# Kernel tuning notes

Hardware: AMD Instinct MI355X
Metric: run time of the kernel (lower is better)

The kernel has to match this reference:

```python
import jax, jax.numpy as jnp
import numpy as np

N_NODES = 100000
N_EDGES = 1600000
IN_DIM = 128
HID = 64


def _init_linear(key, fan_in, fan_out):
    kw, kb = jax.random.split(key)
    bound = 1.0 / np.sqrt(fan_in)
    W = jax.random.uniform(kw, (fan_in, fan_out), jnp.float32, -bound, bound)
    b = jax.random.uniform(kb, (fan_out,), jnp.float32, -bound, bound)
    return W, b


def setup_inputs() -> dict:
    key = jax.random.key(0)
    ks = jax.random.split(key, 6)
    x = jax.random.normal(ks[0], (N_NODES, IN_DIM), jnp.float32)
    edge_index = jax.random.randint(ks[1], (2, N_EDGES), 0, N_NODES, jnp.int64)
    W_pre, b_pre = _init_linear(ks[2], IN_DIM, HID)
    W1, b1 = _init_linear(ks[3], HID, HID)
    W2, b2 = _init_linear(ks[4], HID, HID)
    W3, b3 = _init_linear(ks[5], HID, HID)
    return {"x": x, "edge_index": edge_index, "W_pre": W_pre, "b_pre": b_pre,
            "W1": W1, "b1": b1, "W2": W2, "b2": b2, "W3": W3, "b3": b3}


def _gcn_layer(h, src, dst, dinv, W, b):
    # PyG GCNConv: h' = D^{-1/2} (A + I) D^{-1/2} (h W) + b, deg from A+I
    n = h.shape[0]
    hw = h @ W                                  # [N, out]
    norm = dinv[src] * dinv[dst]                # [E]
    msg = hw[src] * norm[:, None]               # gather + scale  [E, out]
    agg = jax.ops.segment_sum(msg, dst, num_segments=n)  # scatter-add
    agg = agg + hw * (dinv * dinv)[:, None]     # self-loop term (norm = dinv_i^2)
    return agg + b


def reference(x, edge_index, W_pre, b_pre, W1, b1, W2, b2, W3, b3):
    src, dst = edge_index[0], edge_index[1]
    n = x.shape[0]
    # degree of A + I (self loops added, as in GCNConv default)
    deg = jax.ops.segment_sum(jnp.ones(src.shape[0], x.dtype), dst, num_segments=n) + 1.0
    dinv = jax.lax.rsqrt(deg)

    h = x @ W_pre + b_pre                       # feature_pre linear
    h = jax.nn.relu(_gcn_layer(h, src, dst, dinv, W1, b1))  # dropout is identity in eval
    h = jax.nn.relu(_gcn_layer(h, src, dst, dinv, W2, b2))
    h = _gcn_layer(h, src, dst, dinv, W3, b3)
    # F.normalize(p=2, dim=-1) with eps=1e-12
    nrm = jnp.linalg.norm(h, axis=-1, keepdims=True)
    return h / jnp.maximum(nrm, 1e-12)
```

## Files before the change

### kernel.cpp

```cpp
#include <hip/hip_runtime.h>

#define N_NODES 100000
#define N_EDGES 1600000
#define IN_DIM 128
#define HID 64
#define NB 782
#define NT64 1563
#define NGROUP 25000

typedef __attribute__((ext_vector_type(8))) _Float16 h8v;
typedef __attribute__((ext_vector_type(4))) float f4v;

struct Args {
  const float* x; const int* ei;
  const float* Wp; const float* bp;
  const float* W1; const float* b1;
  const float* W2; const float* b2;
  const float* W3; const float* b3;
  float* out;
  _Float16* bufA16; _Float16* hw16;
  int* pairs; int* csr; int* offs; float* dinv;
  int* bsz; int* bboff; int* bcur;
  _Float16* WpH; _Float16* WpL; _Float16* W1H; _Float16* W1L;
  _Float16* W2H; _Float16* W2L; _Float16* W3H; _Float16* W3L;
};

__device__ __forceinline__ void d_split(const float* __restrict__ W,
                                        _Float16* __restrict__ hi,
                                        _Float16* __restrict__ lo, int K, int i) {
  int k = i >> 6, n = i & 63;
  float v = W[i];
  _Float16 h = (_Float16)v;
  float r = v - (float)h;
  hi[n * K + k] = h;
  lo[n * K + k] = (_Float16)r;
}

__global__ __launch_bounds__(256) void f_prep(Args a) {
  int blk = blockIdx.x, t = threadIdx.x;
  if (blk < 32) d_split(a.Wp, a.WpH, a.WpL, IN_DIM, blk * 256 + t);
  else if (blk < 48) d_split(a.W1, a.W1H, a.W1L, HID, (blk - 32) * 256 + t);
  else if (blk < 64) d_split(a.W2, a.W2H, a.W2L, HID, (blk - 48) * 256 + t);
  else d_split(a.W3, a.W3H, a.W3L, HID, (blk - 64) * 256 + t);
}

__global__ __launch_bounds__(256) void f_bhist(Args a) {
  __shared__ int cnt[NB];
  int t = threadIdx.x;
  for (int i = t; i < NB; i += 256) cnt[i] = 0;
  __syncthreads();
  int e0 = blockIdx.x * 8192, e1 = min(e0 + 8192, N_EDGES);
  for (int e = e0 + t; e < e1; e += 256)
    atomicAdd(&cnt[a.ei[N_EDGES + e] >> 7], 1);
  __syncthreads();
  for (int i = t; i < NB; i += 256)
    if (cnt[i]) atomicAdd(&a.bsz[i], cnt[i]);
}

__global__ __launch_bounds__(256) void f_bscan(Args a) {
  __shared__ int sm[256];
  int t = threadIdx.x;
  int c[4];
  int idx0 = t * 4;
#pragma unroll
  for (int j = 0; j < 4; ++j) c[j] = (idx0 + j < NB) ? a.bsz[idx0 + j] : 0;
  int tsum = c[0] + c[1] + c[2] + c[3];
  int val = tsum;
  sm[t] = val;
  __syncthreads();
  for (int off = 1; off < 256; off <<= 1) {
    int u = (t >= off) ? sm[t - off] : 0;
    __syncthreads();
    val += u;
    sm[t] = val;
    __syncthreads();
  }
  int excl = val - tsum;
#pragma unroll
  for (int j = 0; j < 4; ++j) {
    int idx = idx0 + j;
    if (idx < NB) { a.bboff[idx] = excl; a.bcur[idx] = excl; }
    excl += c[j];
  }
  if (t == 255) a.bboff[NB] = val;
}

__global__ __launch_bounds__(256) void f_partition(Args a) {
  __shared__ int cnt[NB];
  __shared__ int base[NB];
  int t = threadIdx.x;
  for (int i = t; i < NB; i += 256) cnt[i] = 0;
  __syncthreads();
  int e0 = blockIdx.x * 8192, e1 = min(e0 + 8192, N_EDGES);
  for (int e = e0 + t; e < e1; e += 256)
    atomicAdd(&cnt[a.ei[N_EDGES + e] >> 7], 1);
  __syncthreads();
  for (int i = t; i < NB; i += 256) {
    int c = cnt[i];
    base[i] = c ? atomicAdd(&a.bcur[i], c) : 0;
    cnt[i] = 0;
  }
  __syncthreads();
  for (int e = e0 + t; e < e1; e += 256) {
    int s = a.ei[e];
    int d = a.ei[N_EDGES + e];
    int b = d >> 7;
    int r = atomicAdd(&cnt[b], 1);
    a.pairs[base[b] + r] = ((d & 127) << 17) | s;
  }
}

__global__ __launch_bounds__(256) void f_csrdeg(Args a) {
  __shared__ int ldeg[128];
  __shared__ int sc[128];
  __shared__ int lcur[128];
  int t = threadIdx.x;
  int b = blockIdx.x;
  int node0 = b << 7;
  int nloc = min(128, N_NODES - node0);
  int beg = a.bboff[b], end = a.bboff[b + 1];
  if (t < 128) ldeg[t] = 0;
  __syncthreads();
  for (int i = beg + t; i < end; i += 256)
    atomicAdd(&ldeg[(a.pairs[i] >> 17) & 127], 1);
  __syncthreads();
  int dv = (t < 128) ? ldeg[t] : 0;
  if (t < 128) sc[t] = dv;
  __syncthreads();
  for (int off = 1; off < 128; off <<= 1) {
    int u = (t >= off && t < 128) ? sc[t - off] : 0;
    __syncthreads();
    if (t < 128) sc[t] += u;
    __syncthreads();
  }
  if (t < nloc) {
    int o = beg + sc[t] - dv;
    a.offs[node0 + t] = o;
    lcur[t] = o;
    a.dinv[node0 + t] = rsqrtf((float)dv + 1.0f);
  }
  if (b == NB - 1 && t == 0) a.offs[N_NODES] = N_EDGES;
  __syncthreads();
  for (int i = beg + t; i < end; i += 256) {
    int p = a.pairs[i];
    int pos = atomicAdd(&lcur[(p >> 17) & 127], 1);
    a.csr[pos] = p & 131071;
  }
}

__global__ __launch_bounds__(256) void f_gemm_pre(Args a) {
  const int K = IN_DIM;
  int wave = threadIdx.x >> 6;
  int lane = threadIdx.x & 63;
  int fi = lane & 15;
  int quad = lane >> 4;
  int r0 = blockIdx.x * 64 + wave * 16;
  int row_l = r0 + fi;
  if (row_l >= N_NODES) row_l = N_NODES - 1;
  const float* xp = a.x + (size_t)row_l * K + quad * 8;

  f4v acc[4];
#pragma unroll
  for (int ct = 0; ct < 4; ++ct) acc[ct] = (f4v){0.f, 0.f, 0.f, 0.f};

#pragma unroll
  for (int k0 = 0; k0 < K; k0 += 32) {
    f4v xa = *(const f4v*)(xp + k0);
    f4v xb = *(const f4v*)(xp + k0 + 4);
    h8v ah, al;
#pragma unroll
    for (int j = 0; j < 4; ++j) {
      _Float16 h = (_Float16)xa[j];
      ah[j] = h;
      al[j] = (_Float16)(xa[j] - (float)h);
    }
#pragma unroll
    for (int j = 0; j < 4; ++j) {
      _Float16 h = (_Float16)xb[j];
      ah[4 + j] = h;
      al[4 + j] = (_Float16)(xb[j] - (float)h);
    }
    const _Float16* whp = a.WpH + (size_t)fi * K + k0 + quad * 8;
    const _Float16* wlp = a.WpL + (size_t)fi * K + k0 + quad * 8;
#pragma unroll
    for (int ct = 0; ct < 4; ++ct) {
      h8v bh = *(const h8v*)(whp + (size_t)ct * 16 * K);
      h8v bl = *(const h8v*)(wlp + (size_t)ct * 16 * K);
      acc[ct] = __builtin_amdgcn_mfma_f32_16x16x32_f16(ah, bh, acc[ct], 0, 0, 0);
      acc[ct] = __builtin_amdgcn_mfma_f32_16x16x32_f16(al, bh, acc[ct], 0, 0, 0);
      acc[ct] = __builtin_amdgcn_mfma_f32_16x16x32_f16(ah, bl, acc[ct], 0, 0, 0);
    }
  }
#pragma unroll
  for (int ct = 0; ct < 4; ++ct) {
    float bv = a.bp[ct * 16 + fi];
#pragma unroll
    for (int j = 0; j < 4; ++j) {
      int orow = r0 + quad * 4 + j;
      if (orow < N_NODES)
        a.bufA16[(size_t)orow * HID + ct * 16 + fi] = (_Float16)(acc[ct][j] + bv);
    }
  }
}

__global__ __launch_bounds__(256) void f_gemm64(Args a, const _Float16* __restrict__ Wh,
                                                const _Float16* __restrict__ Wl) {
  const int K = HID;
  int wave = threadIdx.x >> 6;
  int lane = threadIdx.x & 63;
  int fi = lane & 15;
  int quad = lane >> 4;
  int r0 = blockIdx.x * 64 + wave * 16;
  int row_l = r0 + fi;
  if (row_l >= N_NODES) row_l = N_NODES - 1;
  const _Float16* xp = a.bufA16 + (size_t)row_l * K + quad * 8;

  f4v acc[4];
#pragma unroll
  for (int ct = 0; ct < 4; ++ct) acc[ct] = (f4v){0.f, 0.f, 0.f, 0.f};

#pragma unroll
  for (int k0 = 0; k0 < K; k0 += 32) {
    h8v av = *(const h8v*)(xp + k0);
    const _Float16* whp = Wh + (size_t)fi * K + k0 + quad * 8;
    const _Float16* wlp = Wl + (size_t)fi * K + k0 + quad * 8;
#pragma unroll
    for (int ct = 0; ct < 4; ++ct) {
      h8v bh = *(const h8v*)(whp + (size_t)ct * 16 * K);
      h8v bl = *(const h8v*)(wlp + (size_t)ct * 16 * K);
      acc[ct] = __builtin_amdgcn_mfma_f32_16x16x32_f16(av, bh, acc[ct], 0, 0, 0);
      acc[ct] = __builtin_amdgcn_mfma_f32_16x16x32_f16(av, bl, acc[ct], 0, 0, 0);
    }
  }
#pragma unroll
  for (int ct = 0; ct < 4; ++ct) {
#pragma unroll
    for (int j = 0; j < 4; ++j) {
      int orow = r0 + quad * 4 + j;
      if (orow < N_NODES)
        a.hw16[(size_t)orow * HID + ct * 16 + fi] = (_Float16)acc[ct][j];
    }
  }
}

template <int MODE>
__device__ __forceinline__ void d_agg(int grp, const _Float16* __restrict__ hw,
                                      const int* __restrict__ offs,
                                      const int* __restrict__ csr,
                                      const float* __restrict__ dinv,
                                      const float* __restrict__ bias,
                                      _Float16* __restrict__ out16,
                                      float* __restrict__ out32) {
  int node = grp * 4 + (threadIdx.x >> 6);
  int lane = threadIdx.x & 63;
  int oct = lane >> 3;
  int fi = lane & 7;
  float di = dinv[node];
  int beg = offs[node];
  int end = offs[node + 1];

  float acc[8];
#pragma unroll
  for (int c = 0; c < 8; ++c) acc[c] = 0.f;

  if (oct == 0) {
    h8v hv = *(const h8v*)(hw + (size_t)node * HID + fi * 8);
    float w = di * di;
#pragma unroll
    for (int c = 0; c < 8; ++c) acc[c] += (float)hv[c] * w;
  }
  for (int e0 = beg + oct; e0 < end; e0 += 32) {
    int ss[4];
    float ww[4];
#pragma unroll
    for (int j = 0; j < 4; ++j) {
      int e = e0 + 8 * j;
      bool v = e < end;
      int s = csr[v ? e : beg];
      ss[j] = v ? s : node;
      ww[j] = v ? di : 0.0f;
    }
#pragma unroll
    for (int j = 0; j < 4; ++j) ww[j] *= dinv[ss[j]];
    h8v hv[4];
#pragma unroll
    for (int j = 0; j < 4; ++j)
      hv[j] = *(const h8v*)(hw + (size_t)ss[j] * HID + fi * 8);
#pragma unroll
    for (int j = 0; j < 4; ++j)
#pragma unroll
      for (int c = 0; c < 8; ++c) acc[c] += (float)hv[j][c] * ww[j];
  }
#pragma unroll
  for (int c = 0; c < 8; ++c) {
    float v = acc[c];
    v += __shfl_xor(v, 8);
    v += __shfl_xor(v, 16);
    v += __shfl_xor(v, 32);
    acc[c] = v;
  }
  if (oct == 0) {
#pragma unroll
    for (int c = 0; c < 8; ++c) acc[c] += bias[fi * 8 + c];
    if (MODE == 0) {
      h8v o;
#pragma unroll
      for (int c = 0; c < 8; ++c) o[c] = (_Float16)fmaxf(acc[c], 0.f);
      *(h8v*)(out16 + (size_t)node * HID + fi * 8) = o;
    } else {
      float ss = 0.f;
#pragma unroll
      for (int c = 0; c < 8; ++c) ss += acc[c] * acc[c];
      ss += __shfl_xor(ss, 1);
      ss += __shfl_xor(ss, 2);
      ss += __shfl_xor(ss, 4);
      float sc = 1.0f / fmaxf(sqrtf(ss), 1e-12f);
      f4v o0 = {acc[0] * sc, acc[1] * sc, acc[2] * sc, acc[3] * sc};
      f4v o1 = {acc[4] * sc, acc[5] * sc, acc[6] * sc, acc[7] * sc};
      *(f4v*)(out32 + (size_t)node * HID + fi * 8) = o0;
      *(f4v*)(out32 + (size_t)node * HID + fi * 8 + 4) = o1;
    }
  }
}

__global__ __launch_bounds__(256) void f_agg_relu(Args a, const float* bias) {
  d_agg<0>(blockIdx.x, a.hw16, a.offs, a.csr, a.dinv, bias, a.bufA16, nullptr);
}

__global__ __launch_bounds__(256) void f_agg_norm(Args a) {
  d_agg<1>(blockIdx.x, a.hw16, a.offs, a.csr, a.dinv, a.b3, nullptr, a.out);
}

extern "C" void kernel_launch(void* const* d_in, const int* in_sizes, int n_in,
                              void* d_out, int out_size, void* d_ws, size_t ws_size,
                              hipStream_t stream) {
  char* ws = (char*)d_ws;
  Args a;
  a.x  = (const float*)d_in[0];
  a.ei = (const int*)d_in[1];
  a.Wp = (const float*)d_in[2];  a.bp = (const float*)d_in[3];
  a.W1 = (const float*)d_in[4];  a.b1 = (const float*)d_in[5];
  a.W2 = (const float*)d_in[6];  a.b2 = (const float*)d_in[7];
  a.W3 = (const float*)d_in[8];  a.b3 = (const float*)d_in[9];
  a.out  = (float*)d_out;
  a.bufA16 = (_Float16*)(ws + 0);
  a.hw16   = (_Float16*)(ws + 12800000);
  a.pairs  = (int*)(ws + 25600000);
  a.csr    = (int*)(ws + 32000000);
  a.offs   = (int*)(ws + 38400000);
  a.dinv   = (float*)(ws + 38800016);
  a.bsz    = (int*)(ws + 39200016);
  a.bboff  = (int*)(ws + 39203152);
  a.bcur   = (int*)(ws + 39206288);
  a.WpH = (_Float16*)(ws + 39210000);
  a.WpL = (_Float16*)(ws + 39226384);
  a.W1H = (_Float16*)(ws + 39242768);
  a.W1L = (_Float16*)(ws + 39250960);
  a.W2H = (_Float16*)(ws + 39259152);
  a.W2L = (_Float16*)(ws + 39267344);
  a.W3H = (_Float16*)(ws + 39275536);
  a.W3L = (_Float16*)(ws + 39283728);

  (void)hipMemsetAsync(a.bsz, 0, NB * sizeof(int), stream);
  f_prep<<<80, 256, 0, stream>>>(a);
  f_bhist<<<196, 256, 0, stream>>>(a);
  f_bscan<<<1, 256, 0, stream>>>(a);
  f_partition<<<196, 256, 0, stream>>>(a);
  f_csrdeg<<<NB, 256, 0, stream>>>(a);
  f_gemm_pre<<<NT64, 256, 0, stream>>>(a);
  f_gemm64<<<NT64, 256, 0, stream>>>(a, a.W1H, a.W1L);
  f_agg_relu<<<NGROUP, 256, 0, stream>>>(a, a.b1);
  f_gemm64<<<NT64, 256, 0, stream>>>(a, a.W2H, a.W2L);
  f_agg_relu<<<NGROUP, 256, 0, stream>>>(a, a.b2);
  f_gemm64<<<NT64, 256, 0, stream>>>(a, a.W3H, a.W3L);
  f_agg_norm<<<NGROUP, 256, 0, stream>>>(a);
}
```

Measured before the change: 383.2 us.

## Process two row tiles per wave and stage pre-GEMM weights in LDS

Each wave now computes 32 rows (two 16-row tiles) instead of 16, which halves the block count for the dense GEMMs. The weight fragments are loaded once and reused across both tiles, held in registers for the 64-wide GEMMs and in swizzled shared memory for the input projection. The next tile's activations are prefetched while the current tile's MFMAs run. The aim is to cut redundant weight loads from global memory and hide load latency, at the cost of more registers and LDS per block and fewer blocks.

```diff
diff --git a/kernel.cpp b/kernel.cpp
--- a/kernel.cpp
+++ b/kernel.cpp
@@ -5,7 +5,7 @@
 #define IN_DIM 128
 #define HID 64
 #define NB 782
-#define NT64 1563
+#define NBLK_GEMM 782
 #define NGROUP 25000
 
 typedef __attribute__((ext_vector_type(8))) _Float16 h8v;
@@ -149,97 +149,140 @@
 }
 
 __global__ __launch_bounds__(256) void f_gemm_pre(Args a) {
-  const int K = IN_DIM;
-  int wave = threadIdx.x >> 6;
-  int lane = threadIdx.x & 63;
-  int fi = lane & 15;
-  int quad = lane >> 4;
-  int r0 = blockIdx.x * 64 + wave * 16;
-  int row_l = r0 + fi;
-  if (row_l >= N_NODES) row_l = N_NODES - 1;
-  const float* xp = a.x + (size_t)row_l * K + quad * 8;
-
-  f4v acc[4];
-#pragma unroll
-  for (int ct = 0; ct < 4; ++ct) acc[ct] = (f4v){0.f, 0.f, 0.f, 0.f};
-
-#pragma unroll
-  for (int k0 = 0; k0 < K; k0 += 32) {
-    f4v xa = *(const f4v*)(xp + k0);
-    f4v xb = *(const f4v*)(xp + k0 + 4);
-    h8v ah, al;
+  __shared__ _Float16 sW[2 * 64 * IN_DIM];
+  int t = threadIdx.x;
+  int wave = t >> 6, lane = t & 63, fi = lane & 15, quad = lane >> 4;
+  int r0 = blockIdx.x * 128 + wave * 32;
+
+  f4v xb0[8], xb1[8];
+  {
+    int row = r0 + fi; if (row >= N_NODES) row = N_NODES - 1;
+    const float* xp = a.x + (size_t)row * IN_DIM + quad * 8;
 #pragma unroll
     for (int j = 0; j < 4; ++j) {
-      _Float16 h = (_Float16)xa[j];
-      ah[j] = h;
-      al[j] = (_Float16)(xa[j] - (float)h);
-    }
-#pragma unroll
-    for (int j = 0; j < 4; ++j) {
-      _Float16 h = (_Float16)xb[j];
-      ah[4 + j] = h;
-      al[4 + j] = (_Float16)(xb[j] - (float)h);
-    }
-    const _Float16* whp = a.WpH + (size_t)fi * K + k0 + quad * 8;
-    const _Float16* wlp = a.WpL + (size_t)fi * K + k0 + quad * 8;
+      xb0[2 * j]     = *(const f4v*)(xp + j * 32);
+      xb0[2 * j + 1] = *(const f4v*)(xp + j * 32 + 4);
+    }
+  }
+#pragma unroll
+  for (int i = 0; i < 8; ++i) {
+    int c = i * 256 + t;
+    int h = c >> 10;
+    int c2 = c & 1023;
+    int n = c2 >> 4;
+    const _Float16* src = (h ? a.WpL : a.WpH) + c2 * 8;
+    f4v v = *(const f4v*)src;
+    int off = (h << 14) | ((c2 * 16) ^ ((n & 7) << 4));
+    *(f4v*)((char*)sW + off) = v;
+  }
+  __syncthreads();
+
+  float bv[4];
+#pragma unroll
+  for (int ct = 0; ct < 4; ++ct) bv[ct] = a.bp[ct * 16 + fi];
+
+#pragma unroll
+  for (int f = 0; f < 2; ++f) {
+    f4v* xcur = (f & 1) ? xb1 : xb0;
+    f4v* xnxt = (f & 1) ? xb0 : xb1;
+    if (f < 1) {
+      int row = r0 + 16 + fi; if (row >= N_NODES) row = N_NODES - 1;
+      const float* xp = a.x + (size_t)row * IN_DIM + quad * 8;
+#pragma unroll
+      for (int j = 0; j < 4; ++j) {
+        xnxt[2 * j]     = *(const f4v*)(xp + j * 32);
+        xnxt[2 * j + 1] = *(const f4v*)(xp + j * 32 + 4);
+      }
+    }
+    f4v acc[4];
+#pragma unroll
+    for (int ct = 0; ct < 4; ++ct) acc[ct] = (f4v){0.f, 0.f, 0.f, 0.f};
+#pragma unroll
+    for (int k0i = 0; k0i < 4; ++k0i) {
+      h8v ah, al;
+#pragma unroll
+      for (int j = 0; j < 4; ++j) {
+        float v0 = xcur[2 * k0i][j], v1 = xcur[2 * k0i + 1][j];
+        _Float16 h0 = (_Float16)v0, h1 = (_Float16)v1;
+        ah[j] = h0;     al[j] = (_Float16)(v0 - (float)h0);
+        ah[4 + j] = h1; al[4 + j] = (_Float16)(v1 - (float)h1);
+      }
+#pragma unroll
+      for (int ct = 0; ct < 4; ++ct) {
+        int n = ct * 16 + fi;
+        int bo = ((n * IN_DIM + k0i * 32 + quad * 8) * 2) ^ ((n & 7) << 4);
+        h8v bh = *(const h8v*)((const char*)sW + bo);
+        h8v bl = *(const h8v*)((const char*)sW + 16384 + bo);
+        acc[ct] = __builtin_amdgcn_mfma_f32_16x16x32_f16(ah, bh, acc[ct], 0, 0, 0);
+        acc[ct] = __builtin_amdgcn_mfma_f32_16x16x32_f16(al, bh, acc[ct], 0, 0, 0);
+        acc[ct] = __builtin_amdgcn_mfma_f32_16x16x32_f16(ah, bl, acc[ct], 0, 0, 0);
+      }
+    }
+    int ro = r0 + f * 16;
 #pragma unroll
     for (int ct = 0; ct < 4; ++ct) {
-      h8v bh = *(const h8v*)(whp + (size_t)ct * 16 * K);
-      h8v bl = *(const h8v*)(wlp + (size_t)ct * 16 * K);
-      acc[ct] = __builtin_amdgcn_mfma_f32_16x16x32_f16(ah, bh, acc[ct], 0, 0, 0);
-      acc[ct] = __builtin_amdgcn_mfma_f32_16x16x32_f16(al, bh, acc[ct], 0, 0, 0);
-      acc[ct] = __builtin_amdgcn_mfma_f32_16x16x32_f16(ah, bl, acc[ct], 0, 0, 0);
-    }
-  }
-#pragma unroll
-  for (int ct = 0; ct < 4; ++ct) {
-    float bv = a.bp[ct * 16 + fi];
-#pragma unroll
-    for (int j = 0; j < 4; ++j) {
-      int orow = r0 + quad * 4 + j;
-      if (orow < N_NODES)
-        a.bufA16[(size_t)orow * HID + ct * 16 + fi] = (_Float16)(acc[ct][j] + bv);
+#pragma unroll
+      for (int j = 0; j < 4; ++j) {
+        int orow = ro + quad * 4 + j;
+        if (orow < N_NODES)
+          a.bufA16[(size_t)orow * HID + ct * 16 + fi] = (_Float16)(acc[ct][j] + bv[ct]);
+      }
     }
   }
 }
 
 __global__ __launch_bounds__(256) void f_gemm64(Args a, const _Float16* __restrict__ Wh,
                                                 const _Float16* __restrict__ Wl) {
-  const int K = HID;
-  int wave = threadIdx.x >> 6;
-  int lane = threadIdx.x & 63;
-  int fi = lane & 15;
-  int quad = lane >> 4;
-  int r0 = blockIdx.x * 64 + wave * 16;
-  int row_l = r0 + fi;
-  if (row_l >= N_NODES) row_l = N_NODES - 1;
-  const _Float16* xp = a.bufA16 + (size_t)row_l * K + quad * 8;
-
-  f4v acc[4];
-#pragma unroll
-  for (int ct = 0; ct < 4; ++ct) acc[ct] = (f4v){0.f, 0.f, 0.f, 0.f};
-
-#pragma unroll
-  for (int k0 = 0; k0 < K; k0 += 32) {
-    h8v av = *(const h8v*)(xp + k0);
-    const _Float16* whp = Wh + (size_t)fi * K + k0 + quad * 8;
-    const _Float16* wlp = Wl + (size_t)fi * K + k0 + quad * 8;
+  int t = threadIdx.x;
+  int wave = t >> 6, lane = t & 63, fi = lane & 15, quad = lane >> 4;
+  int r0 = blockIdx.x * 128 + wave * 32;
+
+  h8v a0[2], a1[2];
+  {
+    int row = r0 + fi; if (row >= N_NODES) row = N_NODES - 1;
+    const _Float16* xp = a.bufA16 + (size_t)row * HID + quad * 8;
+    a0[0] = *(const h8v*)xp;
+    a0[1] = *(const h8v*)(xp + 32);
+  }
+  h8v Bh[2][4], Bl[2][4];
+#pragma unroll
+  for (int k0i = 0; k0i < 2; ++k0i)
 #pragma unroll
     for (int ct = 0; ct < 4; ++ct) {
-      h8v bh = *(const h8v*)(whp + (size_t)ct * 16 * K);
-      h8v bl = *(const h8v*)(wlp + (size_t)ct * 16 * K);
-      acc[ct] = __builtin_amdgcn_mfma_f32_16x16x32_f16(av, bh, acc[ct], 0, 0, 0);
-      acc[ct] = __builtin_amdgcn_mfma_f32_16x16x32_f16(av, bl, acc[ct], 0, 0, 0);
-    }
-  }
-#pragma unroll
-  for (int ct = 0; ct < 4; ++ct) {
-#pragma unroll
-    for (int j = 0; j < 4; ++j) {
-      int orow = r0 + quad * 4 + j;
-      if (orow < N_NODES)
-        a.hw16[(size_t)orow * HID + ct * 16 + fi] = (_Float16)acc[ct][j];
-    }
+      size_t o = (size_t)(ct * 16 + fi) * HID + k0i * 32 + quad * 8;
+      Bh[k0i][ct] = *(const h8v*)(Wh + o);
+      Bl[k0i][ct] = *(const h8v*)(Wl + o);
+    }
+
+#pragma unroll
+  for (int f = 0; f < 2; ++f) {
+    h8v* av = (f & 1) ? a1 : a0;
+    h8v* nx = (f & 1) ? a0 : a1;
+    if (f < 1) {
+      int row = r0 + 16 + fi; if (row >= N_NODES) row = N_NODES - 1;
+      const _Float16* xp = a.bufA16 + (size_t)row * HID + quad * 8;
+      nx[0] = *(const h8v*)xp;
+      nx[1] = *(const h8v*)(xp + 32);
+    }
+    f4v acc[4];
+#pragma unroll
+    for (int ct = 0; ct < 4; ++ct) acc[ct] = (f4v){0.f, 0.f, 0.f, 0.f};
+#pragma unroll
+    for (int k0i = 0; k0i < 2; ++k0i)
+#pragma unroll
+      for (int ct = 0; ct < 4; ++ct) {
+        acc[ct] = __builtin_amdgcn_mfma_f32_16x16x32_f16(av[k0i], Bh[k0i][ct], acc[ct], 0, 0, 0);
+        acc[ct] = __builtin_amdgcn_mfma_f32_16x16x32_f16(av[k0i], Bl[k0i][ct], acc[ct], 0, 0, 0);
+      }
+    int ro = r0 + f * 16;
+#pragma unroll
+    for (int ct = 0; ct < 4; ++ct)
+#pragma unroll
+      for (int j = 0; j < 4; ++j) {
+        int orow = ro + quad * 4 + j;
+        if (orow < N_NODES)
+          a.hw16[(size_t)orow * HID + ct * 16 + fi] = (_Float16)acc[ct][j];
+      }
   }
 }
 
@@ -367,11 +410,11 @@
   f_bscan<<<1, 256, 0, stream>>>(a);
   f_partition<<<196, 256, 0, stream>>>(a);
   f_csrdeg<<<NB, 256, 0, stream>>>(a);
-  f_gemm_pre<<<NT64, 256, 0, stream>>>(a);
-  f_gemm64<<<NT64, 256, 0, stream>>>(a, a.W1H, a.W1L);
+  f_gemm_pre<<<NBLK_GEMM, 256, 0, stream>>>(a);
+  f_gemm64<<<NBLK_GEMM, 256, 0, stream>>>(a, a.W1H, a.W1L);
   f_agg_relu<<<NGROUP, 256, 0, stream>>>(a, a.b1);
-  f_gemm64<<<NT64, 256, 0, stream>>>(a, a.W2H, a.W2L);
+  f_gemm64<<<NBLK_GEMM, 256, 0, stream>>>(a, a.W2H, a.W2L);
   f_agg_relu<<<NGROUP, 256, 0, stream>>>(a, a.b2);
-  f_gemm64<<<NT64, 256, 0, stream>>>(a, a.W3H, a.W3L);
+  f_gemm64<<<NBLK_GEMM, 256, 0, stream>>>(a, a.W3H, a.W3L);
   f_agg_norm<<<NGROUP, 256, 0, stream>>>(a);
 }
```

New measurement: 347.3 us. -9.4%, faster.
